# Performance work log

Measured on AMD Instinct MI355X. Metric: run time of the kernel, lower is better.

## Reference

```python
import jax, jax.numpy as jnp
import numpy as np
import math

B, S, D, H, NL, DFF, C, K = 32, 1024, 512, 8, 6, 2048, 128, 8
HD = D // H  # head_dim = 64
EPS = 1e-5


def setup_inputs() -> dict:
    key = jax.random.key(0)
    ks = jax.random.split(key, 24)
    n = lambda k, shape, s=0.02: jax.random.normal(k, shape, jnp.float32) * s
    return {
        'theta': jax.random.uniform(ks[0], (B, S), jnp.float32, -math.pi, math.pi),
        'cond': jax.random.normal(ks[1], (B, C), jnp.float32),
        'attn_bias': jax.random.normal(ks[2], (H, S, S), jnp.float32) * 0.1,
        'embed_W': n(ks[3], (2, D)), 'embed_b': jnp.zeros((D,), jnp.float32),
        'ln1_g': jnp.ones((NL, D), jnp.float32), 'ln1_b': jnp.zeros((NL, D), jnp.float32),
        'ada1_W': n(ks[4], (NL, C, 2 * D)), 'ada1_b': jnp.zeros((NL, 2 * D), jnp.float32),
        'Wq': n(ks[5], (NL, D, D)), 'bq': jnp.zeros((NL, D), jnp.float32),
        'Wk': n(ks[6], (NL, D, D)), 'bk': jnp.zeros((NL, D), jnp.float32),
        'Wv': n(ks[7], (NL, D, D)), 'bv': jnp.zeros((NL, D), jnp.float32),
        'Wo': n(ks[8], (NL, D, D)), 'bo': jnp.zeros((NL, D), jnp.float32),
        'ln2_g': jnp.ones((NL, D), jnp.float32), 'ln2_b': jnp.zeros((NL, D), jnp.float32),
        'ada2_W': n(ks[9], (NL, C, 2 * D)), 'ada2_b': jnp.zeros((NL, 2 * D), jnp.float32),
        'W1': n(ks[10], (NL, D, DFF)), 'b1': jnp.zeros((NL, DFF), jnp.float32),
        'W2': n(ks[11], (NL, DFF, D)), 'b2': jnp.zeros((NL, D), jnp.float32),
        'fn_g': jnp.ones((D,), jnp.float32), 'fn_b': jnp.zeros((D,), jnp.float32),
        'head_W': n(ks[12], (D, 3 * K)), 'head_b': jnp.zeros((3 * K,), jnp.float32),
    }


def _layer_norm(x, g, b):
    m = jnp.mean(x, axis=-1, keepdims=True)
    v = jnp.mean(jnp.square(x - m), axis=-1, keepdims=True)
    return (x - m) * jax.lax.rsqrt(v + EPS) * g + b


def _adaln(x, cond, g, b, pW, pb):
    # AdaLN(x, c) = (1 + scale(c)) * LN(x) + shift(c)
    ss = cond @ pW + pb                      # [B, 2D]
    scale, shift = jnp.split(ss, 2, axis=-1)  # each [B, D]
    return (1.0 + scale[:, None, :]) * _layer_norm(x, g, b) + shift[:, None, :]


def reference(theta, cond, attn_bias, embed_W, embed_b, ln1_g, ln1_b, ada1_W, ada1_b,
              Wq, bq, Wk, bk, Wv, bv, Wo, bo, ln2_g, ln2_b, ada2_W, ada2_b,
              W1, b1, W2, b2, fn_g, fn_b, head_W, head_b):
    b_sz, s_len = theta.shape
    # circular embedding: (cos, sin) -> d_model
    emb_in = jnp.stack([jnp.cos(theta), jnp.sin(theta)], axis=-1)  # [B, S, 2]
    x = emb_in @ embed_W + embed_b                                 # [B, S, D]
    causal = jnp.triu(jnp.ones((s_len, s_len), bool), k=1)         # True above diag
    neg_inf = jnp.asarray(-jnp.inf, x.dtype)
    inv_sqrt = 1.0 / math.sqrt(HD)
    for i in range(NL):
        h = _adaln(x, cond, ln1_g[i], ln1_b[i], ada1_W[i], ada1_b[i])
        q = (h @ Wq[i] + bq[i]).reshape(b_sz, s_len, H, HD)
        k = (h @ Wk[i] + bk[i]).reshape(b_sz, s_len, H, HD)
        v = (h @ Wv[i] + bv[i]).reshape(b_sz, s_len, H, HD)
        scores = jnp.einsum('bqhd,bkhd->bhqk', q, k) * inv_sqrt  # [B, H, S, S]
        scores = scores + attn_bias[None]
        scores = jnp.where(causal[None, None], neg_inf, scores)
        attn = jax.nn.softmax(scores, axis=-1)
        ao = jnp.einsum('bhqk,bkhd->bqhd', attn, v).reshape(b_sz, s_len, D)
        x = x + (ao @ Wo[i] + bo[i])
        h2 = _adaln(x, cond, ln2_g[i], ln2_b[i], ada2_W[i], ada2_b[i])
        ff = jax.nn.gelu(h2 @ W1[i] + b1[i], approximate=False) @ W2[i] + b2[i]
        x = x + ff
    x = _layer_norm(x, fn_g, fn_b)
    return x @ head_W + head_b  # [B, S, 3K] mixture params (logw, mu, log-kappa)
```

## Files before the change

### kernel.cpp

```cpp
#include <hip/hip_runtime.h>


typedef short s8v __attribute__((ext_vector_type(8)));
typedef float f4v __attribute__((ext_vector_type(4)));
typedef unsigned u2v __attribute__((ext_vector_type(2)));
typedef unsigned u4v __attribute__((ext_vector_type(4)));

static __device__ __forceinline__ short f2bf(float f) {
  union { float f; unsigned u; } v; v.f = f;
  unsigned r = v.u + 0x7fffu + ((v.u >> 16) & 1u);
  return (short)(r >> 16);
}
static __device__ __forceinline__ float bf2f(unsigned short s) {
  union { unsigned u; float f; } v; v.u = ((unsigned)s) << 16;
  return v.f;
}
static __device__ __forceinline__ unsigned cvtpk(float lo, float hi) {
  unsigned r;
  asm("v_cvt_pk_bf16_f32 %0, %1, %2" : "=v"(r) : "v"(lo), "v"(hi));
  return r;
}
static __device__ __forceinline__ void gl_lds16(const short* g, short* l) {
  __builtin_amdgcn_global_load_lds(
      (const __attribute__((address_space(1))) unsigned int*)g,
      (__attribute__((address_space(3))) unsigned int*)l, 16, 0, 0);
}

__global__ void transpose_all_k(const float* __restrict__ Wq, const float* __restrict__ Wk,
                                const float* __restrict__ Wv, const float* __restrict__ Wo,
                                const float* __restrict__ W1, const float* __restrict__ W2,
                                int l, short* __restrict__ wbf) {
  int id = blockIdx.x;
  const float* in; short* out; int K, N, tx, ty;
  if (id < 1024) {
    int m = id >> 8, t = id & 255;
    in = (m == 0 ? Wq : m == 1 ? Wk : m == 2 ? Wv : Wo) + (size_t)l * 262144;
    out = wbf + (size_t)m * 262144;
    K = 512; N = 512; tx = t & 15; ty = t >> 4;
  } else if (id < 2048) {
    int t = id - 1024;
    in = W1 + (size_t)l * 1048576; out = wbf + 1048576;
    K = 512; N = 2048; tx = t & 63; ty = t >> 6;
  } else {
    int t = id - 2048;
    in = W2 + (size_t)l * 1048576; out = wbf + 2097152;
    K = 2048; N = 512; tx = t & 15; ty = t >> 4;
  }
  __shared__ float tb[32][33];
  int n0 = tx * 32, k0 = ty * 32;
  int cx = threadIdx.x & 31, cy = threadIdx.x >> 5;
#pragma unroll
  for (int r = 0; r < 4; r++)
    tb[cy + r * 8][cx] = in[(size_t)(k0 + cy + r * 8) * N + n0 + cx];
  __syncthreads();
#pragma unroll
  for (int r = 0; r < 4; r++)
    out[(size_t)(n0 + cy + r * 8) * K + k0 + cx] = f2bf(tb[cx][cy + r * 8]);
}

__global__ void bias_cvt_k(const float* __restrict__ in, short* __restrict__ out) {
  int i = blockIdx.x * 256 + threadIdx.x;
  float4 v = ((const float4*)in)[i];
  ushort4 o;
  o.x = (unsigned short)f2bf(v.x);
  o.y = (unsigned short)f2bf(v.y);
  o.z = (unsigned short)f2bf(v.z);
  o.w = (unsigned short)f2bf(v.w);
  ((ushort4*)out)[i] = o;
}

__global__ void hwt_k(const float* __restrict__ hW, short* __restrict__ hWT) {
  int i = blockIdx.x * 256 + threadIdx.x;
  int n = i >> 9, k = i & 511;
  hWT[i] = (n < 24) ? f2bf(hW[(size_t)k * 24 + n]) : (short)0;
}

__global__ void concat_qkvb_k(const float* bq, const float* bk, const float* bv, float* out) {
  int l = blockIdx.x;
  for (int i = threadIdx.x; i < 1536; i += 256) {
    float v = (i < 512) ? bq[l * 512 + i] * 0.125f
            : (i < 1024 ? bk[l * 512 + i - 512] : bv[l * 512 + i - 1024]);
    out[l * 1536 + i] = v;
  }
}

__global__ void cond_proj_k(const float* __restrict__ cond,
                            const float* __restrict__ a1W, const float* __restrict__ a1b,
                            const float* __restrict__ a2W, const float* __restrict__ a2b,
                            float* __restrict__ ss) {
  int lw = blockIdx.y, which = lw & 1, l = lw >> 1;
  const float* W = (which ? a2W : a1W) + (size_t)l * 128 * 1024;
  const float* bb = (which ? a2b : a1b) + (size_t)l * 1024;
  __shared__ float cs[32 * 128];
  for (int i = threadIdx.x; i < 32 * 128; i += 256) cs[i] = cond[i];
  __syncthreads();
  int n = blockIdx.x * 256 + threadIdx.x;
  float bias = bb[n];
  for (int g = 0; g < 4; g++) {
    float acc[8];
#pragma unroll
    for (int i = 0; i < 8; i++) acc[i] = 0.f;
    for (int c = 0; c < 128; c++) {
      float w = W[(size_t)c * 1024 + n];
#pragma unroll
      for (int i = 0; i < 8; i++) acc[i] += cs[(g * 8 + i) * 128 + c] * w;
    }
#pragma unroll
    for (int i = 0; i < 8; i++)
      ss[((size_t)lw * 32 + g * 8 + i) * 1024 + n] = acc[i] + bias;
  }
}

__global__ void embed_k(const float* __restrict__ theta, const float* __restrict__ eW,
                        const float* __restrict__ eb, float* __restrict__ x) {
  int row = blockIdx.x * 4 + (threadIdx.x >> 6), lane = threadIdx.x & 63;
  float th = theta[row], sn, cn;
  sincosf(th, &sn, &cn);
  int d = lane * 8;
  float* xo = x + (size_t)row * 512 + d;
#pragma unroll
  for (int i = 0; i < 8; i++) xo[i] = cn * eW[d + i] + sn * eW[512 + d + i] + eb[d + i];
}

template<bool HASDEL>
__global__ void adaln_k(float* __restrict__ x, const short* delta,
                        const float* __restrict__ ss,
                        const float* __restrict__ g, const float* __restrict__ be,
                        short* h) {
  int row = blockIdx.x * 4 + (threadIdx.x >> 6), lane = threadIdx.x & 63;
  int b = row >> 10;
  float* xr = x + (size_t)row * 512 + lane * 8;
  float4 va = ((const float4*)xr)[0], vb = ((const float4*)xr)[1];
  float v[8] = {va.x, va.y, va.z, va.w, vb.x, vb.y, vb.z, vb.w};
  if (HASDEL) {
    s8v dv = *(const s8v*)(delta + (size_t)row * 512 + lane * 8);
#pragma unroll
    for (int i = 0; i < 8; i++) v[i] += bf2f((unsigned short)dv[i]);
    float4 o0 = {v[0], v[1], v[2], v[3]}, o1 = {v[4], v[5], v[6], v[7]};
    ((float4*)xr)[0] = o0; ((float4*)xr)[1] = o1;
  }
  float sm = 0.f;
#pragma unroll
  for (int i = 0; i < 8; i++) sm += v[i];
#pragma unroll
  for (int off = 1; off < 64; off <<= 1) sm += __shfl_xor(sm, off);
  float mean = sm * (1.f / 512.f);
  float sq = 0.f;
#pragma unroll
  for (int i = 0; i < 8; i++) { float d = v[i] - mean; sq += d * d; }
#pragma unroll
  for (int off = 1; off < 64; off <<= 1) sq += __shfl_xor(sq, off);
  float rs = rsqrtf(sq * (1.f / 512.f) + 1e-5f);
  const float* sb = ss + (size_t)b * 1024 + lane * 8;
  const float* gp = g + lane * 8;
  const float* bp = be + lane * 8;
  s8v o;
#pragma unroll
  for (int i = 0; i < 8; i++) {
    float xh = (v[i] - mean) * rs * gp[i] + bp[i];
    o[i] = f2bf((1.f + sb[i]) * xh + sb[i + 512]);
  }
  *(s8v*)(h + (size_t)row * 512 + lane * 8) = o;
}

__global__ void fln_k(const float* __restrict__ x, const short* delta,
                      const float* __restrict__ g, const float* __restrict__ be,
                      short* h) {
  int row = blockIdx.x * 4 + (threadIdx.x >> 6), lane = threadIdx.x & 63;
  const float* xr = x + (size_t)row * 512 + lane * 8;
  float4 va = ((const float4*)xr)[0], vb = ((const float4*)xr)[1];
  float v[8] = {va.x, va.y, va.z, va.w, vb.x, vb.y, vb.z, vb.w};
  s8v dv = *(const s8v*)(delta + (size_t)row * 512 + lane * 8);
#pragma unroll
  for (int i = 0; i < 8; i++) v[i] += bf2f((unsigned short)dv[i]);
  float sm = 0.f;
#pragma unroll
  for (int i = 0; i < 8; i++) sm += v[i];
#pragma unroll
  for (int off = 1; off < 64; off <<= 1) sm += __shfl_xor(sm, off);
  float mean = sm * (1.f / 512.f);
  float sq = 0.f;
#pragma unroll
  for (int i = 0; i < 8; i++) { float d = v[i] - mean; sq += d * d; }
#pragma unroll
  for (int off = 1; off < 64; off <<= 1) sq += __shfl_xor(sq, off);
  float rs = rsqrtf(sq * (1.f / 512.f) + 1e-5f);
  const float* gp = g + lane * 8;
  const float* bp = be + lane * 8;
  s8v o;
#pragma unroll
  for (int i = 0; i < 8; i++) o[i] = f2bf((v[i] - mean) * rs * gp[i] + bp[i]);
  *(s8v*)(h + (size_t)row * 512 + lane * 8) = o;
}

template<int EPI>
__global__ __launch_bounds__(256) void gemm_bt_k(const short* __restrict__ A,
                                                 const short* __restrict__ BT,
                                                 const float* __restrict__ bias,
                                                 short* __restrict__ outb,
                                                 int N, int K) {
  __shared__ __align__(16) short lsA[2][4096];
  __shared__ __align__(16) short lsB[2][4096];
  int tid = threadIdx.x, lane = tid & 63, w = tid >> 6;
  int wm = w >> 1, wn = w & 1;
  int l15 = lane & 15, l4 = lane >> 4;
  int lrow = lane >> 2, lchunk = lane & 3;
  int poff = ((l15 << 2) + (l4 ^ ((l15 >> 1) & 3))) << 3;
  int nb = N >> 7;
  int bid = blockIdx.x;
  int xcd = bid & 7, rr = bid >> 3;
  int mloc = rr / nb, nidx = rr - mloc * nb;
  int m0 = (xcd * 32 + mloc) << 7, n0 = nidx << 7;

  f4v z4 = {0.f, 0.f, 0.f, 0.f};
  f4v acc[4][4];
#pragma unroll
  for (int i = 0; i < 4; i++)
#pragma unroll
    for (int j = 0; j < 4; j++) acc[i][j] = z4;

  int co = (lchunk ^ ((lrow >> 1) & 3)) << 3;

  auto STAGE = [&](int t) {
    int slot = t & 1;
    int ko = t << 5;
#pragma unroll
    for (int tt = 0; tt < 2; tt++) {
      int r0 = w * 32 + tt * 16;
      int row = r0 + lrow;
      gl_lds16(A + (size_t)(m0 + row) * K + ko + co, lsA[slot] + r0 * 32);
      gl_lds16(BT + (size_t)(n0 + row) * K + ko + co, lsB[slot] + r0 * 32);
    }
  };

  int NT = K >> 5;
  STAGE(0);
  for (int t = 0; t < NT; ++t) {
    if (t + 1 < NT) {
      STAGE(t + 1);
      asm volatile("s_waitcnt vmcnt(4)" ::: "memory");
    } else {
      asm volatile("s_waitcnt vmcnt(0)" ::: "memory");
    }
    __builtin_amdgcn_s_barrier();
    int slot = t & 1;
    const short* At = lsA[slot] + (wm * 4) * 512 + poff;
    const short* Bt = lsB[slot] + (wn * 4) * 512 + poff;
    s8v af[4], bfr[4];
#pragma unroll
    for (int i = 0; i < 4; i++) {
      af[i] = *(const s8v*)(At + i * 512);
      bfr[i] = *(const s8v*)(Bt + i * 512);
    }
#pragma unroll
    for (int i = 0; i < 4; i++)
#pragma unroll
      for (int j = 0; j < 4; j++)
        acc[i][j] = __builtin_amdgcn_mfma_f32_16x16x32_bf16(af[i], bfr[j], acc[i][j], 0, 0, 0);
    __builtin_amdgcn_s_barrier();
  }
#pragma unroll
  for (int i = 0; i < 4; i++) {
    int gr0 = m0 + wm * 64 + i * 16 + l4 * 4;
#pragma unroll
    for (int j = 0; j < 4; j++) {
      int gc = n0 + wn * 64 + j * 16 + l15;
      float bv = bias[gc];
#pragma unroll
      for (int r = 0; r < 4; r++) {
        float v = acc[i][j][r] + bv;
        if (EPI == 1) {
          float tg = v * (-1.5957691216f - 0.0713548162726f * v * v);
          v = v / (1.f + __expf(tg));
        }
        outb[(size_t)(gr0 + r) * N + gc] = f2bf(v);
      }
    }
  }
}

__global__ __launch_bounds__(256) void qkvt_k(const short* __restrict__ A,
                                              const short* __restrict__ BT,
                                              const float* __restrict__ bias,
                                              short* __restrict__ qk,
                                              short* __restrict__ vtb) {
  __shared__ __align__(16) short lsA[2][4096];
  __shared__ __align__(16) short lsB[2][4096];
  int tid = threadIdx.x, lane = tid & 63, w = tid >> 6;
  int wm = w >> 1, wn = w & 1;
  int l15 = lane & 15, l4 = lane >> 4;
  int lrow = lane >> 2, lchunk = lane & 3;
  int poff = ((l15 << 2) + (l4 ^ ((l15 >> 1) & 3))) << 3;
  int bid = blockIdx.x;
  int xcd = bid & 7, rr = bid >> 3;
  int mloc = rr / 12, nidx = rr - mloc * 12;
  int m0 = (xcd * 32 + mloc) << 7, n0 = nidx << 7;
  bool isV = (n0 >= 1024);
  bool isQ = (n0 < 512);

  f4v z4 = {0.f, 0.f, 0.f, 0.f};
  f4v acc[4][4];
#pragma unroll
  for (int i = 0; i < 4; i++)
#pragma unroll
    for (int j = 0; j < 4; j++) acc[i][j] = z4;

  int co = (lchunk ^ ((lrow >> 1) & 3)) << 3;

  auto STAGE = [&](int t) {
    int slot = t & 1;
    int ko = t << 5;
#pragma unroll
    for (int tt = 0; tt < 2; tt++) {
      int r0 = w * 32 + tt * 16;
      int row = r0 + lrow;
      gl_lds16(A + (size_t)(m0 + row) * 512 + ko + co, lsA[slot] + r0 * 32);
      gl_lds16(BT + (size_t)(n0 + row) * 512 + ko + co, lsB[slot] + r0 * 32);
    }
  };

  const int NT = 16;
  STAGE(0);
  for (int t = 0; t < NT; ++t) {
    if (t + 1 < NT) {
      STAGE(t + 1);
      asm volatile("s_waitcnt vmcnt(4)" ::: "memory");
    } else {
      asm volatile("s_waitcnt vmcnt(0)" ::: "memory");
    }
    __builtin_amdgcn_s_barrier();
    int slot = t & 1;
    const short* At = lsA[slot] + (wm * 4) * 512 + poff;
    const short* Bt = lsB[slot] + (wn * 4) * 512 + poff;
    s8v af[4], bfr[4];
#pragma unroll
    for (int i = 0; i < 4; i++) {
      af[i] = *(const s8v*)(At + i * 512);
      bfr[i] = *(const s8v*)(Bt + i * 512);
    }
    if (!isV) {
#pragma unroll
      for (int i = 0; i < 4; i++)
#pragma unroll
        for (int j = 0; j < 4; j++)
          acc[i][j] = __builtin_amdgcn_mfma_f32_16x16x32_bf16(af[i], bfr[j], acc[i][j], 0, 0, 0);
    } else {
#pragma unroll
      for (int j = 0; j < 4; j++)
#pragma unroll
        for (int i = 0; i < 4; i++)
          acc[j][i] = __builtin_amdgcn_mfma_f32_16x16x32_bf16(bfr[j], af[i], acc[j][i], 0, 0, 0);
    }
    __builtin_amdgcn_s_barrier();
  }
  if (!isV) {
    float scl = isQ ? 0.125f : 1.f;
#pragma unroll
    for (int i = 0; i < 4; i++) {
      int gr0 = m0 + wm * 64 + i * 16 + l4 * 4;
#pragma unroll
      for (int j = 0; j < 4; j++) {
        int gc = n0 + wn * 64 + j * 16 + l15;
        float bv = bias[gc];
#pragma unroll
        for (int r = 0; r < 4; r++)
          qk[(size_t)(gr0 + r) * 1024 + gc] = f2bf(acc[i][j][r] * scl + bv);
      }
    }
  } else {
    int b = m0 >> 10, s0 = m0 & 1023;
#pragma unroll
    for (int j = 0; j < 4; j++) {
      int col = n0 + wn * 64 + j * 16 + l4 * 4;
#pragma unroll
      for (int i = 0; i < 4; i++) {
        int scol = s0 + wm * 64 + i * 16 + l15;
#pragma unroll
        for (int r = 0; r < 4; r++) {
          float v = acc[j][i][r] + bias[col + r];
          vtb[((size_t)b * 512 + col - 1024 + r) * 1024 + scol] = f2bf(v);
        }
      }
    }
  }
}

__global__ __launch_bounds__(256, 4) void attn_k(const short* __restrict__ qk,
                                                 const short* __restrict__ vt,
                                                 const short* __restrict__ biasNT,
                                                 short* __restrict__ ao) {
  __shared__ __align__(16) short Kl[2][64 * 64];
  __shared__ __align__(16) short Vl[2][64 * 64];
  int tid = threadIdx.x, lane = tid & 63, w = tid >> 6;
  int bid = blockIdx.x;
  int qt = 7 - (bid >> 8), b = (bid >> 3) & 31, h = bid & 7;
  int l15 = lane & 15, l4 = lane >> 4;
  int lrow = lane >> 3, lchunk = lane & 7;

  f4v z4 = {0.f, 0.f, 0.f, 0.f};
  s8v qf[2][2];
#pragma unroll
  for (int g = 0; g < 2; g++) {
    const short* qp = qk + (size_t)(b * 1024 + qt * 128 + g * 64 + w * 16 + l15) * 1024 + h * 64;
    qf[g][0] = *(const s8v*)(qp + l4 * 8);
    qf[g][1] = *(const s8v*)(qp + 32 + l4 * 8);
  }
  f4v o[2][4], lac[2];
#pragma unroll
  for (int g = 0; g < 2; g++) {
    lac[g] = z4;
#pragma unroll
    for (int j = 0; j < 4; j++) o[g][j] = z4;
  }
  s8v ones;
#pragma unroll
  for (int e = 0; e < 8; e++) ones[e] = (short)0x3F80;

  auto STAGE = [&](int buf, int kt) {
#pragma unroll
    for (int t = 0; t < 2; t++) {
      int r0 = (w * 2 + t) * 8;
      int row = r0 + lrow;
      gl_lds16(qk + (size_t)(b * 1024 + kt * 64 + row) * 1024 + 512 + h * 64 +
                   ((lchunk ^ (row & 7)) << 3),
               &Kl[buf][r0 * 64]);
      gl_lds16(vt + (size_t)(b * 512 + h * 64 + row) * 1024 + kt * 64 +
                   ((lchunk ^ (row & 7)) << 3),
               &Vl[buf][r0 * 64]);
    }
  };

  int nkt = 2 * qt + 2;
  STAGE(0, 0);
  for (int kt = 0; kt < nkt; kt++) {
    int cur = kt & 1;
    ushort4 bh[2][4];
#pragma unroll
    for (int g = 0; g < 2; g++) {
      if (kt > 2 * qt + g) continue;
      const short* bp = biasNT + ((size_t)h * 1024 + qt * 128 + g * 64 + w * 16 + l15) * 1024 +
                        kt * 64 + l4 * 4;
#pragma unroll
      for (int j = 0; j < 4; j++) bh[g][j] = *(const ushort4*)(bp + j * 16);
    }
    __builtin_amdgcn_sched_barrier(0);
    if (kt + 1 < nkt) {
      STAGE(cur ^ 1, kt + 1);
      asm volatile("s_waitcnt vmcnt(4)" ::: "memory");
    } else {
      asm volatile("s_waitcnt vmcnt(0)" ::: "memory");
    }
    __builtin_amdgcn_s_barrier();
    const short* Kc = &Kl[cur][0];
    const short* Vc = &Vl[cur][0];
#pragma unroll
    for (int g = 0; g < 2; g++) {
      int diag = 2 * qt + g;
      if (kt > diag) continue;
      f4v s[4];
#pragma unroll
      for (int j = 0; j < 4; j++) {
        f4v bc;
        bc[0] = bf2f(bh[g][j].x); bc[1] = bf2f(bh[g][j].y);
        bc[2] = bf2f(bh[g][j].z); bc[3] = bf2f(bh[g][j].w);
        int kr = j * 16 + l15;
        s8v kf0 = *(const s8v*)(Kc + kr * 64 + ((l4 ^ (kr & 7)) << 3));
        s8v kf1 = *(const s8v*)(Kc + kr * 64 + (((l4 + 4) ^ (kr & 7)) << 3));
        s[j] = __builtin_amdgcn_mfma_f32_16x16x32_bf16(kf0, qf[g][0], bc, 0, 0, 0);
        s[j] = __builtin_amdgcn_mfma_f32_16x16x32_bf16(kf1, qf[g][1], s[j], 0, 0, 0);
      }
      if (kt == diag) {
#pragma unroll
        for (int j = 0; j < 4; j++)
#pragma unroll
          for (int r = 0; r < 4; r++) {
            int kk = j * 16 + l4 * 4 + r, qq = w * 16 + l15;
            s[j][r] = (kk > qq) ? 0.f : __expf(s[j][r]);
          }
      } else {
#pragma unroll
        for (int j = 0; j < 4; j++)
#pragma unroll
          for (int r = 0; r < 4; r++) s[j][r] = __expf(s[j][r]);
      }
      unsigned X0[4], X1[4];
#pragma unroll
      for (int j = 0; j < 4; j++) {
        X0[j] = cvtpk(s[j][0], s[j][1]);
        X1[j] = cvtpk(s[j][2], s[j][3]);
      }
      u2v a0 = __builtin_amdgcn_permlane32_swap(X0[0], X0[1], false, false);
      u2v a1 = __builtin_amdgcn_permlane16_swap(a0[0], a0[1], false, false);
      u2v b0 = __builtin_amdgcn_permlane32_swap(X1[0], X1[1], false, false);
      u2v b1 = __builtin_amdgcn_permlane16_swap(b0[0], b0[1], false, false);
      u2v c0 = __builtin_amdgcn_permlane32_swap(X0[2], X0[3], false, false);
      u2v c1 = __builtin_amdgcn_permlane16_swap(c0[0], c0[1], false, false);
      u2v d0 = __builtin_amdgcn_permlane32_swap(X1[2], X1[3], false, false);
      u2v d1 = __builtin_amdgcn_permlane16_swap(d0[0], d0[1], false, false);
      u4v P0 = {a1[0], b1[0], a1[1], b1[1]};
      u4v P1 = {c1[0], d1[0], c1[1], d1[1]};
      s8v pf0 = __builtin_bit_cast(s8v, P0);
      s8v pf1 = __builtin_bit_cast(s8v, P1);
      lac[g] = __builtin_amdgcn_mfma_f32_16x16x32_bf16(pf0, ones, lac[g], 0, 0, 0);
      lac[g] = __builtin_amdgcn_mfma_f32_16x16x32_bf16(pf1, ones, lac[g], 0, 0, 0);
#pragma unroll
      for (int j = 0; j < 4; j++) {
        int dr = j * 16 + l15;
        s8v vf0 = *(const s8v*)(Vc + dr * 64 + ((l4 ^ (dr & 7)) << 3));
        s8v vf1 = *(const s8v*)(Vc + dr * 64 + (((l4 + 4) ^ (dr & 7)) << 3));
        o[g][j] = __builtin_amdgcn_mfma_f32_16x16x32_bf16(pf0, vf0, o[g][j], 0, 0, 0);
        o[g][j] = __builtin_amdgcn_mfma_f32_16x16x32_bf16(pf1, vf1, o[g][j], 0, 0, 0);
      }
    }
    __builtin_amdgcn_s_barrier();
  }
#pragma unroll
  for (int g = 0; g < 2; g++)
#pragma unroll
    for (int r = 0; r < 4; r++) {
      float rl = 1.f / lac[g][r];
      int qr = qt * 128 + g * 64 + w * 16 + l4 * 4 + r;
#pragma unroll
      for (int j = 0; j < 4; j++) {
        int d = j * 16 + l15;
        ao[(size_t)(b * 1024 + qr) * 512 + h * 64 + d] = f2bf(o[g][j][r] * rl);
      }
    }
}

__global__ __launch_bounds__(256) void head_k(const short* __restrict__ X,
                                              const short* __restrict__ hWT,
                                              const float* __restrict__ hb,
                                              float* __restrict__ out) {
  __shared__ __align__(16) short lA[128 * 64];
  int tid = threadIdx.x, lane = tid & 63, w = tid >> 6;
  int l15 = lane & 15, l4 = lane >> 4;
  int lrow = lane >> 3, lchunk = lane & 7;
  int m0 = blockIdx.x * 128;
  f4v z4 = {0.f, 0.f, 0.f, 0.f};
  f4v acc[2][2];
#pragma unroll
  for (int i = 0; i < 2; i++)
#pragma unroll
    for (int j = 0; j < 2; j++) acc[i][j] = z4;

  for (int k0 = 0; k0 < 512; k0 += 64) {
#pragma unroll
    for (int t = 0; t < 4; t++) {
      int r0 = (w * 4 + t) * 8;
      int row = r0 + lrow;
      gl_lds16(X + (size_t)(m0 + row) * 512 + k0 + ((lchunk ^ (row & 7)) << 3), lA + r0 * 64);
    }
    __syncthreads();
#pragma unroll
    for (int kk = 0; kk < 2; kk++) {
      s8v af[2], bfr[2];
#pragma unroll
      for (int i = 0; i < 2; i++) {
        int ra = w * 32 + i * 16 + l15;
        af[i] = *(const s8v*)(lA + ra * 64 + (((l4 + kk * 4) ^ (ra & 7)) << 3));
      }
#pragma unroll
      for (int j = 0; j < 2; j++)
        bfr[j] = *(const s8v*)(hWT + (size_t)(j * 16 + l15) * 512 + k0 + kk * 32 + l4 * 8);
#pragma unroll
      for (int i = 0; i < 2; i++)
#pragma unroll
        for (int j = 0; j < 2; j++)
          acc[i][j] = __builtin_amdgcn_mfma_f32_16x16x32_bf16(af[i], bfr[j], acc[i][j], 0, 0, 0);
    }
    __syncthreads();
  }
#pragma unroll
  for (int i = 0; i < 2; i++) {
#pragma unroll
    for (int j = 0; j < 2; j++) {
      int col = j * 16 + l15;
      if (col < 24) {
        float bv = hb[col];
#pragma unroll
        for (int r = 0; r < 4; r++) {
          int row = m0 + w * 32 + i * 16 + l4 * 4 + r;
          out[(size_t)row * 24 + col] = acc[i][j][r] + bv;
        }
      }
    }
  }
}

extern "C" void kernel_launch(void* const* d_in, const int* in_sizes, int n_in,
                              void* d_out, int out_size, void* d_ws, size_t ws_size,
                              hipStream_t stream) {
  (void)in_sizes; (void)n_in; (void)out_size;
  const float* theta   = (const float*)d_in[0];
  const float* cond    = (const float*)d_in[1];
  const float* attn_b  = (const float*)d_in[2];
  const float* embed_W = (const float*)d_in[3];
  const float* embed_b = (const float*)d_in[4];
  const float* ln1_g   = (const float*)d_in[5];
  const float* ln1_b   = (const float*)d_in[6];
  const float* ada1_W  = (const float*)d_in[7];
  const float* ada1_b  = (const float*)d_in[8];
  const float* Wq      = (const float*)d_in[9];
  const float* bq      = (const float*)d_in[10];
  const float* Wk      = (const float*)d_in[11];
  const float* bk      = (const float*)d_in[12];
  const float* Wv      = (const float*)d_in[13];
  const float* bv      = (const float*)d_in[14];
  const float* Wo      = (const float*)d_in[15];
  const float* bo      = (const float*)d_in[16];
  const float* ln2_g   = (const float*)d_in[17];
  const float* ln2_b   = (const float*)d_in[18];
  const float* ada2_W  = (const float*)d_in[19];
  const float* ada2_b  = (const float*)d_in[20];
  const float* W1      = (const float*)d_in[21];
  const float* b1      = (const float*)d_in[22];
  const float* W2      = (const float*)d_in[23];
  const float* b2      = (const float*)d_in[24];
  const float* fn_g    = (const float*)d_in[25];
  const float* fn_b    = (const float*)d_in[26];
  const float* head_W  = (const float*)d_in[27];
  const float* head_b  = (const float*)d_in[28];

  const size_t REQ = 242814976ull;
  const size_t REQ2 = 259592192ull;
  if (ws_size < REQ) return;
  bool bias_once = (ws_size >= REQ2);

  char* ws = (char*)d_ws;
  float* xw    = (float*)(ws + 0ull);
  short* qk    = (short*)(ws + 67108864ull);
  short* vtb   = (short*)(ws + 134217728ull);
  short* biasT = (short*)(ws + (bias_once ? 242814976ull : 167772160ull));
  short* qf    = (short*)(ws + 67108864ull);
  short* hbuf  = (short*)(ws + 201326592ull);
  short* wbf   = (short*)(ws + 234881024ull);
  float* ssb   = (float*)(ws + 241172480ull);
  float* bqkv  = (float*)(ws + 242745344ull);
  short* hWT   = (short*)(ws + 242782208ull);

  concat_qkvb_k<<<6, 256, 0, stream>>>(bq, bk, bv, bqkv);
  cond_proj_k<<<dim3(4, 12), 256, 0, stream>>>(cond, ada1_W, ada1_b, ada2_W, ada2_b, ssb);
  hwt_k<<<64, 256, 0, stream>>>(head_W, hWT);
  embed_k<<<8192, 256, 0, stream>>>(theta, embed_W, embed_b, xw);
  if (bias_once) bias_cvt_k<<<8192, 256, 0, stream>>>(attn_b, biasT);

  for (int l = 0; l < 6; l++) {
    transpose_all_k<<<3072, 256, 0, stream>>>(Wq, Wk, Wv, Wo, W1, W2, l, wbf);
    if (!bias_once) bias_cvt_k<<<8192, 256, 0, stream>>>(attn_b, biasT);

    if (l == 0)
      adaln_k<false><<<8192, 256, 0, stream>>>(xw, nullptr, ssb + (size_t)(l * 2) * 32768,
                                               ln1_g + l * 512, ln1_b + l * 512, hbuf);
    else
      adaln_k<true><<<8192, 256, 0, stream>>>(xw, hbuf, ssb + (size_t)(l * 2) * 32768,
                                              ln1_g + l * 512, ln1_b + l * 512, hbuf);
    qkvt_k<<<3072, 256, 0, stream>>>(hbuf, wbf, bqkv + l * 1536, qk, vtb);
    attn_k<<<2048, 256, 0, stream>>>(qk, vtb, biasT, hbuf);
    gemm_bt_k<0><<<1024, 256, 0, stream>>>(hbuf, wbf + 786432, bo + l * 512, vtb, 512, 512);
    adaln_k<true><<<8192, 256, 0, stream>>>(xw, vtb, ssb + (size_t)(l * 2 + 1) * 32768,
                                            ln2_g + l * 512, ln2_b + l * 512, hbuf);
    gemm_bt_k<1><<<4096, 256, 0, stream>>>(hbuf, wbf + 1048576, b1 + l * 2048, qf, 2048, 512);
    gemm_bt_k<0><<<1024, 256, 0, stream>>>(qf, wbf + 2097152, b2 + l * 512, hbuf, 512, 2048);
  }
  fln_k<<<8192, 256, 0, stream>>>(xw, hbuf, fn_g, fn_b, hbuf);
  head_k<<<256, 256, 0, stream>>>(hbuf, hWT, head_b, (float*)d_out);
}
```

Before: 2.827 ms.

## Triple-buffer GEMM pipeline, use exp2 in attention, and set MFMA priority

The generic bf16 GEMM moves from a double-buffered to a triple-buffered LDS ring that prefetches two k-tiles ahead. It also loads the next tile's fragments after a single barrier per iteration, so global loads overlap more with MFMA work. Attention softmax switches to the native v_exp_f32 (exp2): the Q scale and the attention bias are pre-multiplied by log2(e), which drops the per-element multiply hidden inside __expf. s_setprio is raised around the MFMA sections of the attention loop to favour matrix issue across waves. The extra LDS buffer raises shared memory per block and may cut occupancy.

```diff
diff --git a/kernel.cpp b/kernel.cpp
--- a/kernel.cpp
+++ b/kernel.cpp
@@ -6,6 +6,9 @@
 typedef unsigned u2v __attribute__((ext_vector_type(2)));
 typedef unsigned u4v __attribute__((ext_vector_type(4)));
 
+#define Q_SCALE 0.18033688011112042f
+#define LOG2E   1.4426950408889634f
+
 static __device__ __forceinline__ short f2bf(float f) {
   union { float f; unsigned u; } v; v.f = f;
   unsigned r = v.u + 0x7fffu + ((v.u >> 16) & 1u);
@@ -18,6 +21,11 @@
 static __device__ __forceinline__ unsigned cvtpk(float lo, float hi) {
   unsigned r;
   asm("v_cvt_pk_bf16_f32 %0, %1, %2" : "=v"(r) : "v"(lo), "v"(hi));
+  return r;
+}
+static __device__ __forceinline__ float fexp2(float x) {
+  float r;
+  asm("v_exp_f32 %0, %1" : "=v"(r) : "v"(x));
   return r;
 }
 static __device__ __forceinline__ void gl_lds16(const short* g, short* l) {
@@ -62,10 +70,10 @@
   int i = blockIdx.x * 256 + threadIdx.x;
   float4 v = ((const float4*)in)[i];
   ushort4 o;
-  o.x = (unsigned short)f2bf(v.x);
-  o.y = (unsigned short)f2bf(v.y);
-  o.z = (unsigned short)f2bf(v.z);
-  o.w = (unsigned short)f2bf(v.w);
+  o.x = (unsigned short)f2bf(v.x * LOG2E);
+  o.y = (unsigned short)f2bf(v.y * LOG2E);
+  o.z = (unsigned short)f2bf(v.z * LOG2E);
+  o.w = (unsigned short)f2bf(v.w * LOG2E);
   ((ushort4*)out)[i] = o;
 }
 
@@ -78,7 +86,7 @@
 __global__ void concat_qkvb_k(const float* bq, const float* bk, const float* bv, float* out) {
   int l = blockIdx.x;
   for (int i = threadIdx.x; i < 1536; i += 256) {
-    float v = (i < 512) ? bq[l * 512 + i] * 0.125f
+    float v = (i < 512) ? bq[l * 512 + i] * Q_SCALE
             : (i < 1024 ? bk[l * 512 + i - 512] : bv[l * 512 + i - 1024]);
     out[l * 1536 + i] = v;
   }
@@ -194,13 +202,13 @@
 }
 
 template<int EPI>
-__global__ __launch_bounds__(256) void gemm_bt_k(const short* __restrict__ A,
-                                                 const short* __restrict__ BT,
-                                                 const float* __restrict__ bias,
-                                                 short* __restrict__ outb,
-                                                 int N, int K) {
-  __shared__ __align__(16) short lsA[2][4096];
-  __shared__ __align__(16) short lsB[2][4096];
+__global__ __launch_bounds__(256, 3) void gemm_r3_k(const short* __restrict__ A,
+                                                    const short* __restrict__ BT,
+                                                    const float* __restrict__ bias,
+                                                    short* __restrict__ outb,
+                                                    int N, int K) {
+  __shared__ __align__(16) short lsA[3][4096];
+  __shared__ __align__(16) short lsB[3][4096];
   int tid = threadIdx.x, lane = tid & 63, w = tid >> 6;
   int wm = w >> 1, wn = w & 1;
   int l15 = lane & 15, l4 = lane >> 4;
@@ -222,7 +230,7 @@
   int co = (lchunk ^ ((lrow >> 1) & 3)) << 3;
 
   auto STAGE = [&](int t) {
-    int slot = t & 1;
+    int slot = t % 3;
     int ko = t << 5;
 #pragma unroll
     for (int tt = 0; tt < 2; tt++) {
@@ -232,32 +240,37 @@
       gl_lds16(BT + (size_t)(n0 + row) * K + ko + co, lsB[slot] + r0 * 32);
     }
   };
-
-  int NT = K >> 5;
-  STAGE(0);
-  for (int t = 0; t < NT; ++t) {
-    if (t + 1 < NT) {
-      STAGE(t + 1);
-      asm volatile("s_waitcnt vmcnt(4)" ::: "memory");
-    } else {
-      asm volatile("s_waitcnt vmcnt(0)" ::: "memory");
-    }
-    __builtin_amdgcn_s_barrier();
-    int slot = t & 1;
+  auto LOADF = [&](int t, s8v* af, s8v* bfr) {
+    int slot = t % 3;
     const short* At = lsA[slot] + (wm * 4) * 512 + poff;
     const short* Bt = lsB[slot] + (wn * 4) * 512 + poff;
-    s8v af[4], bfr[4];
 #pragma unroll
     for (int i = 0; i < 4; i++) {
       af[i] = *(const s8v*)(At + i * 512);
       bfr[i] = *(const s8v*)(Bt + i * 512);
     }
+  };
+
+  int NT = K >> 5;
+  STAGE(0); STAGE(1);
+  asm volatile("s_waitcnt vmcnt(4)" ::: "memory");
+  __builtin_amdgcn_s_barrier();
+  s8v af[4], bfr[4];
+  LOADF(0, af, bfr);
+  for (int t = 0; t < NT; ++t) {
+    if (t + 2 < NT) STAGE(t + 2);
+    __builtin_amdgcn_sched_barrier(0);
 #pragma unroll
     for (int i = 0; i < 4; i++)
 #pragma unroll
       for (int j = 0; j < 4; j++)
         acc[i][j] = __builtin_amdgcn_mfma_f32_16x16x32_bf16(af[i], bfr[j], acc[i][j], 0, 0, 0);
-    __builtin_amdgcn_s_barrier();
+    if (t + 1 < NT) {
+      if (t + 2 < NT) asm volatile("s_waitcnt vmcnt(4)" ::: "memory");
+      else            asm volatile("s_waitcnt vmcnt(0)" ::: "memory");
+      __builtin_amdgcn_s_barrier();
+      LOADF(t + 1, af, bfr);
+    }
   }
 #pragma unroll
   for (int i = 0; i < 4; i++) {
@@ -354,7 +367,7 @@
     __builtin_amdgcn_s_barrier();
   }
   if (!isV) {
-    float scl = isQ ? 0.125f : 1.f;
+    float scl = isQ ? Q_SCALE : 1.f;
 #pragma unroll
     for (int i = 0; i < 4; i++) {
       int gr0 = m0 + wm * 64 + i * 16 + l4 * 4;
@@ -458,6 +471,7 @@
       int diag = 2 * qt + g;
       if (kt > diag) continue;
       f4v s[4];
+      __builtin_amdgcn_s_setprio(1);
 #pragma unroll
       for (int j = 0; j < 4; j++) {
         f4v bc;
@@ -469,19 +483,20 @@
         s[j] = __builtin_amdgcn_mfma_f32_16x16x32_bf16(kf0, qf[g][0], bc, 0, 0, 0);
         s[j] = __builtin_amdgcn_mfma_f32_16x16x32_bf16(kf1, qf[g][1], s[j], 0, 0, 0);
       }
+      __builtin_amdgcn_s_setprio(0);
       if (kt == diag) {
 #pragma unroll
         for (int j = 0; j < 4; j++)
 #pragma unroll
           for (int r = 0; r < 4; r++) {
             int kk = j * 16 + l4 * 4 + r, qq = w * 16 + l15;
-            s[j][r] = (kk > qq) ? 0.f : __expf(s[j][r]);
+            s[j][r] = (kk > qq) ? 0.f : fexp2(s[j][r]);
           }
       } else {
 #pragma unroll
         for (int j = 0; j < 4; j++)
 #pragma unroll
-          for (int r = 0; r < 4; r++) s[j][r] = __expf(s[j][r]);
+          for (int r = 0; r < 4; r++) s[j][r] = fexp2(s[j][r]);
       }
       unsigned X0[4], X1[4];
 #pragma unroll
@@ -501,6 +516,7 @@
       u4v P1 = {c1[0], d1[0], c1[1], d1[1]};
       s8v pf0 = __builtin_bit_cast(s8v, P0);
       s8v pf1 = __builtin_bit_cast(s8v, P1);
+      __builtin_amdgcn_s_setprio(1);
       lac[g] = __builtin_amdgcn_mfma_f32_16x16x32_bf16(pf0, ones, lac[g], 0, 0, 0);
       lac[g] = __builtin_amdgcn_mfma_f32_16x16x32_bf16(pf1, ones, lac[g], 0, 0, 0);
 #pragma unroll
@@ -511,6 +527,7 @@
         o[g][j] = __builtin_amdgcn_mfma_f32_16x16x32_bf16(pf0, vf0, o[g][j], 0, 0, 0);
         o[g][j] = __builtin_amdgcn_mfma_f32_16x16x32_bf16(pf1, vf1, o[g][j], 0, 0, 0);
       }
+      __builtin_amdgcn_s_setprio(0);
     }
     __builtin_amdgcn_s_barrier();
   }
@@ -657,11 +674,11 @@
                                               ln1_g + l * 512, ln1_b + l * 512, hbuf);
     qkvt_k<<<3072, 256, 0, stream>>>(hbuf, wbf, bqkv + l * 1536, qk, vtb);
     attn_k<<<2048, 256, 0, stream>>>(qk, vtb, biasT, hbuf);
-    gemm_bt_k<0><<<1024, 256, 0, stream>>>(hbuf, wbf + 786432, bo + l * 512, vtb, 512, 512);
+    gemm_r3_k<0><<<1024, 256, 0, stream>>>(hbuf, wbf + 786432, bo + l * 512, vtb, 512, 512);
     adaln_k<true><<<8192, 256, 0, stream>>>(xw, vtb, ssb + (size_t)(l * 2 + 1) * 32768,
                                             ln2_g + l * 512, ln2_b + l * 512, hbuf);
-    gemm_bt_k<1><<<4096, 256, 0, stream>>>(hbuf, wbf + 1048576, b1 + l * 2048, qf, 2048, 512);
-    gemm_bt_k<0><<<1024, 256, 0, stream>>>(qf, wbf + 2097152, b2 + l * 512, hbuf, 512, 2048);
+    gemm_r3_k<1><<<4096, 256, 0, stream>>>(hbuf, wbf + 1048576, b1 + l * 2048, qf, 2048, 512);
+    gemm_r3_k<0><<<1024, 256, 0, stream>>>(qf, wbf + 2097152, b2 + l * 512, hbuf, 512, 2048);
   }
   fln_k<<<8192, 256, 0, stream>>>(xw, hbuf, fn_g, fn_b, hbuf);
   head_k<<<256, 256, 0, stream>>>(hbuf, hWT, head_b, (float*)d_out);
```

After: 2.744 ms. -3.0%, faster.
